# Kernel optimization log

Hardware: AMD Instinct MI355X
Metric: run time of the kernel (lower is better)

The kernel has to match this reference:

```python
import jax, jax.numpy as jnp
import numpy as np

R = 16            # DFL bins (reg_max)
C = 80            # num classes
STRIDES = (8, 16, 32)
CONF = 0.25
IOU_T = 0.45
MAX_DET = 300
K_PRE = 1024      # fixed pre-NMS candidate count (static-shape stand-in for torch's boolean mask)
CLS_OFFSET = 4096.0  # > max image coord; class-aware NMS offset (torchvision batched_nms trick)


def setup_inputs() -> dict:
    key = jax.random.key(0)
    k0, k1, k2 = jax.random.split(key, 3)
    B, CH = 16, 4 * R + C
    return {
        "p0": jax.random.normal(k0, (B, CH, 80, 80), jnp.float32),
        "p1": jax.random.normal(k1, (B, CH, 40, 40), jnp.float32),
        "p2": jax.random.normal(k2, (B, CH, 20, 20), jnp.float32),
        "h_img": 640,
        "w_img": 640,
    }


def _decode_level(p, stride):
    # p: (B, 4R+C, H, W)
    B, _, H, W = p.shape
    box_logits = p[:, : 4 * R].reshape(B, 4, R, H * W)
    bins = jnp.arange(R, dtype=p.dtype)
    # DFLIntegral: softmax over bins, expectation -> l,t,r,b distances (in stride units)
    ltrb = jnp.einsum('bkrm,r->bkm', jax.nn.softmax(box_logits, axis=2), bins) * stride  # (B,4,HW)
    yv, xv = jnp.meshgrid(jnp.arange(H, dtype=p.dtype), jnp.arange(W, dtype=p.dtype), indexing='ij')
    cx = (xv.reshape(-1) + 0.5) * stride  # (HW,)
    cy = (yv.reshape(-1) + 0.5) * stride
    x1 = cx[None] - ltrb[:, 0]
    y1 = cy[None] - ltrb[:, 1]
    x2 = cx[None] + ltrb[:, 2]
    y2 = cy[None] + ltrb[:, 3]
    boxes = jnp.stack((x1, y1, x2, y2), axis=2)  # (B, HW, 4)
    scores = jax.nn.sigmoid(p[:, 4 * R:].reshape(B, C, H * W))  # (B, C, HW)
    smax = scores.max(axis=1)      # (B, HW)
    labels = scores.argmax(axis=1)  # (B, HW) int
    return boxes, smax, labels


def _pairwise_iou(b):
    # b: (K, 4) xyxy
    area = (b[:, 2] - b[:, 0]) * (b[:, 3] - b[:, 1])
    lt = jnp.maximum(b[:, None, :2], b[None, :, :2])
    rb = jnp.minimum(b[:, None, 2:], b[None, :, 2:])
    wh = jnp.clip(rb - lt, 0.0)
    inter = wh[..., 0] * wh[..., 1]
    return inter / (area[:, None] + area[None, :] - inter + 1e-7)


def _nms_single(boxes, smax, labels):
    # boxes (A,4), smax (A,), labels (A,)
    s = jnp.where(smax > CONF, smax, -1.0)
    sv, idx = jax.lax.top_k(s, K_PRE)          # score-sorted pre-NMS candidates
    bsel = boxes[idx]                           # (K,4)
    lsel = labels[idx]
    vsel = sv > CONF                            # candidate passes conf filter
    boff = bsel + lsel[:, None].astype(bsel.dtype) * CLS_OFFSET  # class-aware offset
    iou = _pairwise_iou(boff)
    iou = iou * (1.0 - jnp.eye(K_PRE, dtype=iou.dtype))  # no self-suppression

    def step(supp, i):
        keep_i = jnp.logical_and(~supp[i], vsel[i])
        supp = jnp.where(keep_i, supp | (iou[i] > IOU_T), supp)
        return supp, keep_i

    _, keep = jax.lax.scan(step, jnp.zeros(K_PRE, bool), jnp.arange(K_PRE))
    rank = jnp.cumsum(keep) - 1
    slot = jnp.where(keep & (rank < MAX_DET), rank, MAX_DET)  # dump overflow into dummy slot
    boxes_out = jnp.zeros((MAX_DET + 1, 4), bsel.dtype).at[slot].set(bsel)[:MAX_DET]
    scores_out = jnp.zeros((MAX_DET + 1,), sv.dtype).at[slot].set(sv)[:MAX_DET]
    labels_out = jnp.full((MAX_DET + 1,), -1, jnp.int32).at[slot].set(lsel.astype(jnp.int32))[:MAX_DET]
    n = jnp.minimum(keep.sum(), MAX_DET)
    valid_out = jnp.arange(MAX_DET) < n
    return boxes_out, scores_out, labels_out, valid_out


def reference(p0, p1, p2, h_img, w_img):
    parts = [_decode_level(p, s) for p, s in zip((p0, p1, p2), STRIDES)]
    boxes = jnp.concatenate([x[0] for x in parts], axis=1)   # (B, A, 4)
    smax = jnp.concatenate([x[1] for x in parts], axis=1)    # (B, A)
    labels = jnp.concatenate([x[2] for x in parts], axis=1)  # (B, A)
    hi = jnp.array([w_img - 1, h_img - 1, w_img - 1, h_img - 1], boxes.dtype)
    boxes = jnp.clip(boxes, 0.0, hi)
    return jax.vmap(_nms_single)(boxes, smax, labels)
```

## Files before the change

### kernel.cpp

```cpp
#include <hip/hip_runtime.h>
#include <stdint.h>

#define NR 16
#define NC 80
#define NA 8400
#define NB 16
#define KPRE 1024
#define MAXDET 300
#define CONF_T 0.25f
#define IOU_THR 0.45f

__device__ __forceinline__ float read_dim(const void* p) {
  int iv = *(const int*)p;
  return (iv > 0 && iv < (1 << 20)) ? (float)iv : *(const float*)p;
}

__device__ __forceinline__ const float* level_ptr(const float* p0, const float* p1,
                                                  const float* p2, int a, int& HW,
                                                  int& W, float& stride, int& m) {
  if (a < 6400)      { HW = 6400; W = 80; stride = 8.f;  m = a;        return p0; }
  else if (a < 8000) { HW = 1600; W = 40; stride = 16.f; m = a - 6400; return p1; }
  else               { HW = 400;  W = 20; stride = 32.f; m = a - 8000; return p2; }
}

__device__ __forceinline__ uint64_t readlane64(uint64_t v, int lane) {
  uint32_t lo = (uint32_t)__builtin_amdgcn_readlane((int)(uint32_t)v, lane);
  uint32_t hi = (uint32_t)__builtin_amdgcn_readlane((int)(uint32_t)(v >> 32), lane);
  return ((uint64_t)hi << 32) | lo;
}

__global__ __launch_bounds__(256) void k_decode(
    const float* __restrict__ p0, const float* __restrict__ p1,
    const float* __restrict__ p2, const void* __restrict__ hp,
    const void* __restrict__ wp, float4* __restrict__ boxes,
    uint32_t* __restrict__ keys, int* __restrict__ labels) {
  int gid = blockIdx.x * 256 + threadIdx.x;
  int aid = gid >> 2, k = gid & 3;
  int b = aid / NA, a = aid - b * NA;
  int HW, W, m; float stride;
  const float* p = level_ptr(p0, p1, p2, a, HW, W, stride, m);
  const float* base = p + (size_t)b * (4 * NR + NC) * HW + m;

  float v[NR]; float mx = -3.4e38f;
#pragma unroll
  for (int r = 0; r < NR; ++r) { v[r] = base[(size_t)(k * NR + r) * HW]; mx = fmaxf(mx, v[r]); }
  float se = 0.f, sn = 0.f;
#pragma unroll
  for (int r = 0; r < NR; ++r) { float e = expf(v[r] - mx); se += e; sn += e * (float)r; }
  float dk = sn / se * stride;

  float ml = -3.4e38f; int mc = NC;
#pragma unroll 4
  for (int c = 0; c < 20; ++c) {
    int ch = 4 * c + k;
    float vv = base[(size_t)(4 * NR + ch) * HW];
    if (vv > ml) { ml = vv; mc = ch; }
  }
#pragma unroll
  for (int off = 1; off < 4; off <<= 1) {
    float ov = __shfl_xor(ml, off);
    int oc = __shfl_xor(mc, off);
    if (ov > ml || (ov == ml && oc < mc)) { ml = ov; mc = oc; }
  }
  int lane = threadIdx.x & 63;
  int bl = lane & ~3;
  float dl = __shfl(dk, bl), dt = __shfl(dk, bl + 1);
  float dr = __shfl(dk, bl + 2), db = __shfl(dk, bl + 3);

  if (k == 0) {
    int x = m % W, y = m / W;
    float cx = ((float)x + 0.5f) * stride, cy = ((float)y + 0.5f) * stride;
    float hx = read_dim(wp) - 1.f, hy = read_dim(hp) - 1.f;
    boxes[aid] = make_float4(fminf(fmaxf(cx - dl, 0.f), hx),
                             fminf(fmaxf(cy - dt, 0.f), hy),
                             fminf(fmaxf(cx + dr, 0.f), hx),
                             fminf(fmaxf(cy + db, 0.f), hy));
  } else if (k == 1) {
    float smax = 1.f / (1.f + expf(-ml));
    float s = smax > CONF_T ? smax : -1.0f;
    uint32_t bt = __float_as_uint(s);
    keys[aid] = (bt & 0x80000000u) ? ~bt : (bt | 0x80000000u);
  } else if (k == 2) {
    labels[aid] = mc;
  }
}

__global__ __launch_bounds__(1024) void k_selcomp(const uint32_t* __restrict__ keys,
                                                  uint64_t* __restrict__ cmp,
                                                  int* __restrict__ ccount) {
  __shared__ __align__(16) uint32_t skeys[NA];
  __shared__ uint32_t whist[16][256];
  __shared__ uint32_t hsum[256], ssuf[256];
  __shared__ int s_b1, s_rem, s_t16, s_cnt;
  int img = blockIdx.x, tid = threadIdx.x;
  int w = tid >> 6, lane = tid & 63;
  const uint4* kb4 = (const uint4*)(keys + (size_t)img * NA);
  for (int j = tid; j < NA / 4; j += 1024) ((uint4*)skeys)[j] = kb4[j];
  if (tid == 0) s_cnt = 0;

  for (int j = tid; j < 16 * 256; j += 1024) ((uint32_t*)whist)[j] = 0;
  __syncthreads();
  for (int j = tid; j < NA; j += 1024) atomicAdd(&whist[w][skeys[j] >> 24], 1u);
  __syncthreads();
  if (tid < 256) { uint32_t s = 0; for (int i = 0; i < 16; ++i) s += whist[i][tid]; hsum[tid] = s; }
  __syncthreads();
  if (tid < 256) { uint32_t s = 0; for (int j = tid; j < 256; ++j) s += hsum[j]; ssuf[tid] = s; }
  __syncthreads();
  if (tid < 256) {
    uint32_t ab = (tid == 255) ? 0u : ssuf[tid + 1];
    if (ssuf[tid] >= KPRE && ab < KPRE) { s_b1 = tid; s_rem = KPRE - (int)ab; }
  }
  __syncthreads();
  int b1 = s_b1, rem = s_rem;
  __syncthreads();

  for (int j = tid; j < 16 * 256; j += 1024) ((uint32_t*)whist)[j] = 0;
  __syncthreads();
  for (int j = tid; j < NA; j += 1024) {
    uint32_t k = skeys[j];
    if ((int)(k >> 24) == b1) atomicAdd(&whist[w][(k >> 16) & 0xFF], 1u);
  }
  __syncthreads();
  if (tid < 256) { uint32_t s = 0; for (int i = 0; i < 16; ++i) s += whist[i][tid]; hsum[tid] = s; }
  __syncthreads();
  if (tid < 256) { uint32_t s = 0; for (int j = tid; j < 256; ++j) s += hsum[j]; ssuf[tid] = s; }
  __syncthreads();
  if (tid < 256) {
    int ab = (tid == 255) ? 0 : (int)ssuf[tid + 1];
    if ((int)ssuf[tid] >= rem && ab < rem) s_t16 = (b1 << 8) | tid;
  }
  __syncthreads();
  uint32_t t16 = (uint32_t)s_t16;

  for (int j0 = 0; j0 < NA; j0 += 1024) {
    int j = j0 + tid;
    uint32_t k = (j < NA) ? skeys[j] : 0;
    bool pass = (j < NA) && ((k >> 16) >= t16);
    uint64_t mask = __ballot(pass);
    int pre = __popcll(mask & ((1ull << lane) - 1ull));
    int wc = __popcll(mask);
    int base = 0;
    if (lane == 0) base = wc ? atomicAdd(&s_cnt, wc) : 0;
    base = __shfl(base, 0);
    if (pass)
      cmp[(size_t)img * NA + base + pre] =
          ((uint64_t)k << 32) | (uint64_t)(0xFFFFFFFFu - (uint32_t)j);
  }
  __syncthreads();
  if (tid == 0) ccount[img] = s_cnt;
}

__global__ __launch_bounds__(256) void k_rank2(
    const uint64_t* __restrict__ cmp, const int* __restrict__ ccount,
    const float4* __restrict__ boxes, const int* __restrict__ labels,
    float4* __restrict__ selbox, float4* __restrict__ selboff,
    float* __restrict__ selscore, int* __restrict__ sellab) {
  __shared__ uint64_t sk[2048];
  int img = blockIdx.y;
  int M = ccount[img]; if (M > NA) M = NA;
  if (blockIdx.x * 256 >= M) return;
  int c = blockIdx.x * 256 + threadIdx.x;
  uint64_t kc = (c < M) ? cmp[(size_t)img * NA + c] : 0;
  int rank = 0;
  for (int j0 = 0; j0 < M; j0 += 2048) {
    int nchunk = min(2048, M - j0);
    __syncthreads();
    for (int j = threadIdx.x; j < nchunk; j += 256)
      sk[j] = cmp[(size_t)img * NA + j0 + j];
    __syncthreads();
    if (c < M) {
      int j = 0;
      for (; j + 4 <= nchunk; j += 4) {
        rank += (int)(sk[j] > kc) + (int)(sk[j + 1] > kc) +
                (int)(sk[j + 2] > kc) + (int)(sk[j + 3] > kc);
      }
      for (; j < nchunk; ++j) rank += (int)(sk[j] > kc);
    }
  }
  if (c < M && rank < KPRE) {
    int a = (int)(0xFFFFFFFFu - (uint32_t)kc);
    uint32_t uk = (uint32_t)(kc >> 32);
    uint32_t bits = (uk & 0x80000000u) ? (uk & 0x7FFFFFFFu) : ~uk;
    float s = __uint_as_float(bits);
    int lab = labels[img * NA + a];
    float4 bx = boxes[img * NA + a];
    float off = (float)lab * 4096.0f;
    int o = img * KPRE + rank;
    selbox[o] = bx;
    selboff[o] = make_float4(bx.x + off, bx.y + off, bx.z + off, bx.w + off);
    selscore[o] = s;
    sellab[o] = lab;
  }
}

__global__ __launch_bounds__(256) void k_iou(const float4* __restrict__ selboff,
                                             uint64_t* __restrict__ rowmask) {
  __shared__ float4 bb[KPRE];
  int img = blockIdx.y;
  for (int j = threadIdx.x; j < KPRE; j += 256) bb[j] = selboff[img * KPRE + j];
  __syncthreads();
  int i = blockIdx.x * 16 + (threadIdx.x & 15);
  int w = threadIdx.x >> 4;
  int rot = w & 3;
  float4 bi = bb[i];
  float ai = (bi.z - bi.x) * (bi.w - bi.y);
  uint64_t bits = 0;
  for (int jj = 0; jj < 64; ++jj) {
    int jb = (jj + rot) & 63;
    int j = w * 64 + jb;
    float4 bj = bb[j];
    float lx = fmaxf(bi.x, bj.x), ly = fmaxf(bi.y, bj.y);
    float rx = fminf(bi.z, bj.z), ry = fminf(bi.w, bj.w);
    float iw = fmaxf(rx - lx, 0.f), ih = fmaxf(ry - ly, 0.f);
    float inter = iw * ih;
    float aj = (bj.z - bj.x) * (bj.w - bj.y);
    float iou = inter / (ai + aj - inter + 1e-7f);
    bits |= (uint64_t)((iou > IOU_THR) && (j != i)) << jb;
  }
  rowmask[(size_t)img * 16384 + (size_t)w * 1024 + i] = bits;
}

__global__ __launch_bounds__(64) void k_scan(
    const uint64_t* __restrict__ rowmask, const float4* __restrict__ selbox,
    const float* __restrict__ selscore, const int* __restrict__ sellab,
    float* __restrict__ out) {
  __shared__ float lsc[KPRE];
  __shared__ uint64_t buf[2][16 * 65];
  __shared__ int keepidx[MAXDET];
  int img = blockIdx.x, lane = threadIdx.x;
  const uint64_t* g = rowmask + (size_t)img * 16384;

  for (int j = lane; j < KPRE; j += 64) lsc[j] = selscore[img * KPRE + j];

  {
    uint64_t r0[16];
#pragma unroll
    for (int t = 0; t < 16; ++t) r0[t] = g[t * 1024 + lane];
#pragma unroll
    for (int t = 0; t < 16; ++t) buf[0][t * 65 + lane] = r0[t];
  }
  asm volatile("" ::: "memory");

  uint64_t remv = 0;
  int n = 0;
  for (int c = 0; c < 16; ++c) {
    uint64_t rn[16];
    if (c + 1 < 16) {
#pragma unroll
      for (int t = 0; t < 16; ++t) rn[t] = g[t * 1024 + (c + 1) * 64 + lane];
    }
    const uint64_t* B = buf[c & 1];
    uint64_t m = B[c * 65 + lane];
    float sc = lsc[c * 64 + lane];
    uint64_t vmask = __ballot(sc > CONF_T);
    uint64_t cur = readlane64(remv, c);
    uint64_t kmask = 0;
#pragma unroll
    for (int ii = 0; ii < 64; ++ii) {
      if (((vmask >> ii) & 1ull) && !((cur >> ii) & 1ull)) {
        cur |= readlane64(m, ii);
        kmask |= (1ull << ii);
        if (lane == 0 && n < MAXDET) keepidx[n] = c * 64 + ii;
        n++;
      }
    }
    if (lane < 16) {
      uint64_t km = kmask;
      while (km) {
        int ii2 = __ffsll((unsigned long long)km) - 1;
        km &= km - 1;
        remv |= B[lane * 65 + ii2];
      }
    }
    if (!((vmask >> 63) & 1ull) || n >= MAXDET) break;
    if (c + 1 < 16) {
#pragma unroll
      for (int t = 0; t < 16; ++t) buf[(c + 1) & 1][t * 65 + lane] = rn[t];
    }
    asm volatile("" ::: "memory");
  }

  asm volatile("" ::: "memory");
  float* ob = out;
  float* os = out + NB * MAXDET * 4;
  float* ol = out + NB * MAXDET * 5;
  float* ov = out + NB * MAXDET * 6;
  int nk = n < MAXDET ? n : MAXDET;
  for (int s0 = 0; s0 < MAXDET; s0 += 64) {
    int slot = s0 + lane;
    if (slot >= MAXDET) break;
    bool v = slot < nk;
    float4 bx = make_float4(0.f, 0.f, 0.f, 0.f);
    float scv = 0.f, lbv = -1.f;
    if (v) {
      int i = keepidx[slot];
      bx = selbox[img * KPRE + i];
      scv = lsc[i];
      lbv = (float)sellab[img * KPRE + i];
    }
    ((float4*)ob)[img * MAXDET + slot] = bx;
    os[img * MAXDET + slot] = scv;
    ol[img * MAXDET + slot] = lbv;
    ov[img * MAXDET + slot] = v ? 1.0f : 0.0f;
  }
}

extern "C" void kernel_launch(void* const* d_in, const int* in_sizes, int n_in,
                              void* d_out, int out_size, void* d_ws, size_t ws_size,
                              hipStream_t stream) {
  const float* p0 = (const float*)d_in[0];
  const float* p1 = (const float*)d_in[1];
  const float* p2 = (const float*)d_in[2];
  const void* hp = d_in[3];
  const void* wp = d_in[4];

  char* ws = (char*)d_ws;
  float4*   boxes    = (float4*)(ws + 0);
  uint64_t* rowmask  = (uint64_t*)(ws + 0);
  uint32_t* keys     = (uint32_t*)(ws + 2150400);
  int*      labels   = (int*)(ws + 2688000);
  float4*   selbox   = (float4*)(ws + 3225600);
  float4*   selboff  = (float4*)(ws + 3487744);
  float*    selscore = (float*)(ws + 3749888);
  int*      sellab   = (int*)(ws + 3815424);
  int*      ccount   = (int*)(ws + 3880960);
  uint64_t* cmp      = (uint64_t*)(ws + 3881024);

  k_decode<<<(NB * NA * 4) / 256, 256, 0, stream>>>(p0, p1, p2, hp, wp,
                                                    boxes, keys, labels);
  k_selcomp<<<NB, 1024, 0, stream>>>(keys, cmp, ccount);
  dim3 rg((NA + 255) / 256, NB);
  k_rank2<<<rg, 256, 0, stream>>>(cmp, ccount, boxes, labels,
                                  selbox, selboff, selscore, sellab);
  dim3 ig(KPRE / 16, NB);
  k_iou<<<ig, 256, 0, stream>>>(selboff, rowmask);
  k_scan<<<NB, 64, 0, stream>>>(rowmask, selbox, selscore, sellab,
                                (float*)d_out);
}
```

Measured before the change: 206.7 us.

## Fuse top-K selection and rank into one kernel, split NMS mask accumulation across lanes

Merges the candidate-compaction kernel and the rank kernel into one per-image block. Candidates are kept in shared memory up to a cap, with global spill past it, which removes a launch and the global round-trip of the compacted keys. It also precomputes box areas in shared memory for the IoU kernel. In the NMS scan, suppression-row ORs are spread over all 64 lanes in four groups instead of 16, then combined with readlane. The trade-off is that the fused rank step runs on only 16 blocks of 1024 threads, where before it ran across many blocks.

```diff
diff --git a/kernel.cpp b/kernel.cpp
--- a/kernel.cpp
+++ b/kernel.cpp
@@ -9,6 +9,7 @@
 #define MAXDET 300
 #define CONF_T 0.25f
 #define IOU_THR 0.45f
+#define CAP 2048
 
 __device__ __forceinline__ float read_dim(const void* p) {
   int iv = *(const int*)p;
@@ -85,12 +86,15 @@
   }
 }
 
-__global__ __launch_bounds__(1024) void k_selcomp(const uint32_t* __restrict__ keys,
-                                                  uint64_t* __restrict__ cmp,
-                                                  int* __restrict__ ccount) {
+__global__ __launch_bounds__(1024) void k_selrank(
+    const uint32_t* __restrict__ keys, const float4* __restrict__ boxes,
+    const int* __restrict__ labels, uint64_t* __restrict__ cmp,
+    float4* __restrict__ selbox, float4* __restrict__ selboff,
+    float* __restrict__ selscore, int* __restrict__ sellab) {
   __shared__ __align__(16) uint32_t skeys[NA];
   __shared__ uint32_t whist[16][256];
   __shared__ uint32_t hsum[256], ssuf[256];
+  __shared__ uint64_t scmp[CAP];
   __shared__ int s_b1, s_rem, s_t16, s_cnt;
   int img = blockIdx.x, tid = threadIdx.x;
   int w = tid >> 6, lane = tid & 63;
@@ -142,68 +146,61 @@
     int base = 0;
     if (lane == 0) base = wc ? atomicAdd(&s_cnt, wc) : 0;
     base = __shfl(base, 0);
-    if (pass)
-      cmp[(size_t)img * NA + base + pre] =
-          ((uint64_t)k << 32) | (uint64_t)(0xFFFFFFFFu - (uint32_t)j);
-  }
-  __syncthreads();
-  if (tid == 0) ccount[img] = s_cnt;
-}
-
-__global__ __launch_bounds__(256) void k_rank2(
-    const uint64_t* __restrict__ cmp, const int* __restrict__ ccount,
-    const float4* __restrict__ boxes, const int* __restrict__ labels,
-    float4* __restrict__ selbox, float4* __restrict__ selboff,
-    float* __restrict__ selscore, int* __restrict__ sellab) {
-  __shared__ uint64_t sk[2048];
-  int img = blockIdx.y;
-  int M = ccount[img]; if (M > NA) M = NA;
-  if (blockIdx.x * 256 >= M) return;
-  int c = blockIdx.x * 256 + threadIdx.x;
-  uint64_t kc = (c < M) ? cmp[(size_t)img * NA + c] : 0;
-  int rank = 0;
-  for (int j0 = 0; j0 < M; j0 += 2048) {
-    int nchunk = min(2048, M - j0);
-    __syncthreads();
-    for (int j = threadIdx.x; j < nchunk; j += 256)
-      sk[j] = cmp[(size_t)img * NA + j0 + j];
-    __syncthreads();
-    if (c < M) {
-      int j = 0;
-      for (; j + 4 <= nchunk; j += 4) {
-        rank += (int)(sk[j] > kc) + (int)(sk[j + 1] > kc) +
-                (int)(sk[j + 2] > kc) + (int)(sk[j + 3] > kc);
-      }
-      for (; j < nchunk; ++j) rank += (int)(sk[j] > kc);
-    }
-  }
-  if (c < M && rank < KPRE) {
-    int a = (int)(0xFFFFFFFFu - (uint32_t)kc);
-    uint32_t uk = (uint32_t)(kc >> 32);
-    uint32_t bits = (uk & 0x80000000u) ? (uk & 0x7FFFFFFFu) : ~uk;
-    float s = __uint_as_float(bits);
-    int lab = labels[img * NA + a];
-    float4 bx = boxes[img * NA + a];
-    float off = (float)lab * 4096.0f;
-    int o = img * KPRE + rank;
-    selbox[o] = bx;
-    selboff[o] = make_float4(bx.x + off, bx.y + off, bx.z + off, bx.w + off);
-    selscore[o] = s;
-    sellab[o] = lab;
+    if (pass) {
+      int slot = base + pre;
+      uint64_t v = ((uint64_t)k << 32) | (uint64_t)(0xFFFFFFFFu - (uint32_t)j);
+      if (slot < CAP) scmp[slot] = v;
+      else cmp[(size_t)img * NA + slot] = v;
+    }
+  }
+  __threadfence_block();
+  __syncthreads();
+
+  int M = s_cnt; if (M > NA) M = NA;
+  int lim = M < CAP ? M : CAP;
+  for (int c = tid; c < M; c += 1024) {
+    uint64_t kc = (c < CAP) ? scmp[c] : cmp[(size_t)img * NA + c];
+    int rank = 0;
+    int j = 0;
+    for (; j + 4 <= lim; j += 4) {
+      rank += (int)(scmp[j] > kc) + (int)(scmp[j + 1] > kc) +
+              (int)(scmp[j + 2] > kc) + (int)(scmp[j + 3] > kc);
+    }
+    for (; j < lim; ++j) rank += (int)(scmp[j] > kc);
+    for (j = CAP; j < M; ++j) rank += (int)(cmp[(size_t)img * NA + j] > kc);
+    if (rank < KPRE) {
+      int a = (int)(0xFFFFFFFFu - (uint32_t)kc);
+      uint32_t uk = (uint32_t)(kc >> 32);
+      uint32_t bits = (uk & 0x80000000u) ? (uk & 0x7FFFFFFFu) : ~uk;
+      float s = __uint_as_float(bits);
+      int lab = labels[img * NA + a];
+      float4 bx = boxes[(size_t)img * NA + a];
+      float off = (float)lab * 4096.0f;
+      int o = img * KPRE + rank;
+      selbox[o] = bx;
+      selboff[o] = make_float4(bx.x + off, bx.y + off, bx.z + off, bx.w + off);
+      selscore[o] = s;
+      sellab[o] = lab;
+    }
   }
 }
 
 __global__ __launch_bounds__(256) void k_iou(const float4* __restrict__ selboff,
                                              uint64_t* __restrict__ rowmask) {
   __shared__ float4 bb[KPRE];
+  __shared__ float sar[KPRE];
   int img = blockIdx.y;
-  for (int j = threadIdx.x; j < KPRE; j += 256) bb[j] = selboff[img * KPRE + j];
+  for (int j = threadIdx.x; j < KPRE; j += 256) {
+    float4 v = selboff[img * KPRE + j];
+    bb[j] = v;
+    sar[j] = (v.z - v.x) * (v.w - v.y);
+  }
   __syncthreads();
   int i = blockIdx.x * 16 + (threadIdx.x & 15);
   int w = threadIdx.x >> 4;
   int rot = w & 3;
   float4 bi = bb[i];
-  float ai = (bi.z - bi.x) * (bi.w - bi.y);
+  float ai = sar[i];
   uint64_t bits = 0;
   for (int jj = 0; jj < 64; ++jj) {
     int jb = (jj + rot) & 63;
@@ -213,7 +210,7 @@
     float rx = fminf(bi.z, bj.z), ry = fminf(bi.w, bj.w);
     float iw = fmaxf(rx - lx, 0.f), ih = fmaxf(ry - ly, 0.f);
     float inter = iw * ih;
-    float aj = (bj.z - bj.x) * (bj.w - bj.y);
+    float aj = sar[j];
     float iou = inter / (ai + aj - inter + 1e-7f);
     bits |= (uint64_t)((iou > IOU_THR) && (j != i)) << jb;
   }
@@ -228,6 +225,7 @@
   __shared__ uint64_t buf[2][16 * 65];
   __shared__ int keepidx[MAXDET];
   int img = blockIdx.x, lane = threadIdx.x;
+  int wsel = lane & 15, sub = lane >> 4;
   const uint64_t* g = rowmask + (size_t)img * 16384;
 
   for (int j = lane; j < KPRE; j += 64) lsc[j] = selscore[img * KPRE + j];
@@ -253,7 +251,8 @@
     uint64_t m = B[c * 65 + lane];
     float sc = lsc[c * 64 + lane];
     uint64_t vmask = __ballot(sc > CONF_T);
-    uint64_t cur = readlane64(remv, c);
+    uint64_t cur = readlane64(remv, c) | readlane64(remv, c + 16) |
+                   readlane64(remv, c + 32) | readlane64(remv, c + 48);
     uint64_t kmask = 0;
 #pragma unroll
     for (int ii = 0; ii < 64; ++ii) {
@@ -262,17 +261,21 @@
         kmask |= (1ull << ii);
         if (lane == 0 && n < MAXDET) keepidx[n] = c * 64 + ii;
         n++;
+        if (n >= MAXDET) break;
       }
     }
-    if (lane < 16) {
+    bool done = !((vmask >> 63) & 1ull) || n >= MAXDET;
+    if (!done) {
       uint64_t km = kmask;
+      int t = 0;
       while (km) {
         int ii2 = __ffsll((unsigned long long)km) - 1;
         km &= km - 1;
-        remv |= B[lane * 65 + ii2];
+        if ((t & 3) == sub) remv |= B[wsel * 65 + ii2];
+        ++t;
       }
     }
-    if (!((vmask >> 63) & 1ull) || n >= MAXDET) break;
+    if (done) break;
     if (c + 1 < 16) {
 #pragma unroll
       for (int t = 0; t < 16; ++t) buf[(c + 1) & 1][t * 65 + lane] = rn[t];
@@ -323,15 +326,12 @@
   float4*   selboff  = (float4*)(ws + 3487744);
   float*    selscore = (float*)(ws + 3749888);
   int*      sellab   = (int*)(ws + 3815424);
-  int*      ccount   = (int*)(ws + 3880960);
   uint64_t* cmp      = (uint64_t*)(ws + 3881024);
 
   k_decode<<<(NB * NA * 4) / 256, 256, 0, stream>>>(p0, p1, p2, hp, wp,
                                                     boxes, keys, labels);
-  k_selcomp<<<NB, 1024, 0, stream>>>(keys, cmp, ccount);
-  dim3 rg((NA + 255) / 256, NB);
-  k_rank2<<<rg, 256, 0, stream>>>(cmp, ccount, boxes, labels,
-                                  selbox, selboff, selscore, sellab);
+  k_selrank<<<NB, 1024, 0, stream>>>(keys, boxes, labels, cmp,
+                                     selbox, selboff, selscore, sellab);
   dim3 ig(KPRE / 16, NB);
   k_iou<<<ig, 256, 0, stream>>>(selboff, rowmask);
   k_scan<<<NB, 64, 0, stream>>>(rowmask, selbox, selscore, sellab,
```

New measurement: 238.5 us. +15.4%, slower.
